# Optimization experiments

Measured on AMD Instinct MI355X. Metric: run time of the kernel, lower is better.

Reference implementation:

```python
import jax, jax.numpy as jnp
import numpy as np

DIM = 2048
BATCH = 64


def setup_inputs() -> dict:
    key = jax.random.key(0)
    kx, kq, kk, kv = jax.random.split(key, 4)
    s = 1.0 / np.sqrt(DIM).astype(np.float32)  # keep q*k logits O(1)
    x = jax.random.normal(kx, (BATCH, DIM), dtype=jnp.float32)
    Wq = jax.random.normal(kq, (DIM, DIM), dtype=jnp.float32) * s
    Wk = jax.random.normal(kk, (DIM, DIM), dtype=jnp.float32) * s
    Wv = jax.random.normal(kv, (DIM, DIM), dtype=jnp.float32) * s
    return {"x": x, "Wq": Wq, "Wk": Wk, "Wv": Wv}


def reference(x, Wq, Wk, Wv):
    # nn.Linear(dim, inner_dim, bias=False): y = x @ W.T, W: [inner_dim, dim]
    q = x @ Wq.T  # [b, N]  (head_dim = 1, so each token's q is a scalar)
    k = x @ Wk.T  # [b, N]
    v = x @ Wv.T  # [b, N]
    # dot[b,i,j] = q[b,i] * k[b,j]  (rank-1 outer product per batch)
    logits = q[:, :, None] * k[:, None, :]  # [b, N, N]
    attn = jax.nn.softmax(logits, axis=-1)
    out = jnp.einsum("bij,bj->bi", attn, v)  # [b, N]
    # dim == inner_dim -> scale is Identity
    return out
```

## Files before the change

### kernel.cpp

```cpp
#include <hip/hip_runtime.h>
#include <hip/hip_bf16.h>

#define DIM 2048
#define NB  64
#define KSL 4
#define JSL 8

typedef short bf16x8 __attribute__((ext_vector_type(8)));
typedef short s16x4  __attribute__((ext_vector_type(4)));
typedef float f32x4  __attribute__((ext_vector_type(4)));
typedef float f32x2  __attribute__((ext_vector_type(2)));

__device__ __forceinline__ unsigned short f32_to_bf16_rne(float f) {
  unsigned u = __builtin_bit_cast(unsigned, f);
  unsigned r = u + 0x7FFF + ((u >> 16) & 1);
  return (unsigned short)(r >> 16);
}

__global__ __launch_bounds__(256)
void prep(const float* __restrict__ x, unsigned short* __restrict__ xrh,
          unsigned short* __restrict__ xrl) {
  const int tg = blockIdx.x * 256 + threadIdx.x;
  const int b = tg >> 9;
  const int k = (tg & 511) * 4;
  float4 f = *(const float4*)(x + (size_t)b * DIM + k);
  const int mt = b >> 4, l15 = b & 15;
  const int ck = k >> 5, quad = (k >> 3) & 3, u = k & 7;
  const size_t off = (((size_t)(mt * 64 + ck) * 64) + quad * 16 + l15) * 8 + u;
  float vf[4] = {f.x, f.y, f.z, f.w};
  ushort4 h4, l4;
  unsigned short* hp = &h4.x;
  unsigned short* lp = &l4.x;
#pragma unroll
  for (int e = 0; e < 4; ++e) {
    unsigned short h = f32_to_bf16_rne(vf[e]);
    float hf = __builtin_bit_cast(float, ((unsigned)h) << 16);
    hp[e] = h;
    lp[e] = f32_to_bf16_rne(vf[e] - hf);
  }
  *(ushort4*)(xrh + off) = h4;
  *(ushort4*)(xrl + off) = l4;
}

#define WSTR 260

__device__ __forceinline__ void conv_store_w(short (*wh)[WSTR], short (*wl)[WSTR],
                                             const float4* wreg, int wave, int lane) {
#pragma unroll
  for (int p = 0; p < 8; ++p) {
    const int r = p * 4 + wave;
    float wf[4] = {wreg[p].x, wreg[p].y, wreg[p].z, wreg[p].w};
    s16x4 h4, l4;
#pragma unroll
    for (int e = 0; e < 4; ++e) {
      unsigned uu = __builtin_bit_cast(unsigned, wf[e]);
      h4[e] = (short)(uu >> 16);
      float hf = __builtin_bit_cast(float, uu & 0xFFFF0000u);
      float res = wf[e] - hf;
      l4[e] = (short)(__builtin_bit_cast(unsigned, res) >> 16);
    }
    *(s16x4*)&wh[r][lane * 4] = h4;
    *(s16x4*)&wl[r][lane * 4] = l4;
  }
}

__global__ __launch_bounds__(256)
void qkv_mfma(const unsigned short* __restrict__ xrh,
              const unsigned short* __restrict__ xrl,
              const float* __restrict__ Wq, const float* __restrict__ Wk,
              const float* __restrict__ Wv, float* __restrict__ part) {
  const int mat = blockIdx.z;
  const float* __restrict__ W = (mat == 0) ? Wq : ((mat == 1) ? Wk : Wv);
  const int t = threadIdx.x;
  const int wave = t >> 6, lane = t & 63;
  const int l15 = lane & 15, quad = lane >> 4;
  const int j0 = blockIdx.x * 32;
  const int kb0 = blockIdx.y * 512;

  __shared__ __align__(16) short wh[32][WSTR];
  __shared__ __align__(16) short wl[32][WSTR];

  const int jh = wave & 1;
  const int mh = wave >> 1;
  const int frow = jh * 16 + l15;
  f32x4 acc[2] = {{0.f,0.f,0.f,0.f},{0.f,0.f,0.f,0.f}};

  float4 wa[8], wb[8];
#pragma unroll
  for (int p = 0; p < 8; ++p)
    wa[p] = *(const float4*)(W + (size_t)(j0 + p * 4 + wave) * DIM + kb0 + lane * 4);

#pragma unroll
  for (int c = 0; c < 2; ++c) {
    if (c == 0) conv_store_w(wh, wl, wa, wave, lane);
    else        conv_store_w(wh, wl, wb, wave, lane);
    if (c == 0) {
#pragma unroll
      for (int p = 0; p < 8; ++p)
        wb[p] = *(const float4*)(W + (size_t)(j0 + p * 4 + wave) * DIM +
                                 kb0 + 256 + lane * 4);
    }
    __syncthreads();

    const int ckb = blockIdx.y * 16 + c * 8;
#pragma unroll
    for (int kk = 0; kk < 8; ++kk) {
      bf16x8 whf, wlf;
      *(s16x4*)&whf       = *(const s16x4*)&wh[frow][kk * 32 + quad * 8];
      *(((s16x4*)&whf)+1) = *(const s16x4*)&wh[frow][kk * 32 + quad * 8 + 4];
      *(s16x4*)&wlf       = *(const s16x4*)&wl[frow][kk * 32 + quad * 8];
      *(((s16x4*)&wlf)+1) = *(const s16x4*)&wl[frow][kk * 32 + quad * 8 + 4];
      const int ck = ckb + kk;
#pragma unroll
      for (int u = 0; u < 2; ++u) {
        const int mt = mh * 2 + u;
        const size_t xo = (((size_t)(mt * 64 + ck)) * 64 + lane) * 8;
        bf16x8 ah = *(const bf16x8*)(xrh + xo);
        bf16x8 al = *(const bf16x8*)(xrl + xo);
        acc[u] = __builtin_amdgcn_mfma_f32_16x16x32_bf16(ah, whf, acc[u], 0, 0, 0);
        acc[u] = __builtin_amdgcn_mfma_f32_16x16x32_bf16(al, whf, acc[u], 0, 0, 0);
        acc[u] = __builtin_amdgcn_mfma_f32_16x16x32_bf16(ah, wlf, acc[u], 0, 0, 0);
      }
    }
    if (c == 0) __syncthreads();
  }

  float* __restrict__ pb =
      part + ((size_t)(blockIdx.y * 3 + mat) * NB) * DIM + j0 + jh * 16 + l15;
#pragma unroll
  for (int u = 0; u < 2; ++u)
#pragma unroll
    for (int r = 0; r < 4; ++r) {
      const int b = (mh * 2 + u) * 16 + quad * 4 + r;
      pb[(size_t)b * DIM] = acc[u][r];
    }
}

__global__ __launch_bounds__(256)
void attn(const float* __restrict__ part, f32x2* __restrict__ pnd) {
  const int b = blockIdx.z, js = blockIdx.y, t = threadIdx.x;
  const int i0 = blockIdx.x * 512;
  const int ia = i0 + t, ib = i0 + 256 + t;
  const int jb = js * (DIM / JSL);

  __shared__ __align__(16) float ks[DIM / JSL];
  __shared__ __align__(16) float vs[DIM / JSL];

  float kv = 0.f, vv = 0.f, qa = 0.f, qb = 0.f;
#pragma unroll
  for (int sl = 0; sl < KSL; ++sl) {
    kv += part[((size_t)(sl * 3 + 1) * NB + b) * DIM + jb + t];
    vv += part[((size_t)(sl * 3 + 2) * NB + b) * DIM + jb + t];
    qa += part[((size_t)(sl * 3 + 0) * NB + b) * DIM + ia];
    qb += part[((size_t)(sl * 3 + 0) * NB + b) * DIM + ib];
  }
  ks[t] = kv;
  vs[t] = vv;
  __syncthreads();

  const float ca = qa * 1.4426950408889634f;
  const float cb = qb * 1.4426950408889634f;
  const f32x2 ca2 = {ca, ca}, cb2 = {cb, cb};

  f32x2 na0 = {0.f,0.f}, na1 = {0.f,0.f}, da0 = {0.f,0.f}, da1 = {0.f,0.f};
  f32x2 nb0 = {0.f,0.f}, nb1 = {0.f,0.f}, db0 = {0.f,0.f}, db1 = {0.f,0.f};
#pragma unroll 4
  for (int j = 0; j < DIM / JSL; j += 8) {
    f32x2 k01 = *(const f32x2*)(ks + j);
    f32x2 k23 = *(const f32x2*)(ks + j + 2);
    f32x2 k45 = *(const f32x2*)(ks + j + 4);
    f32x2 k67 = *(const f32x2*)(ks + j + 6);
    f32x2 v01 = *(const f32x2*)(vs + j);
    f32x2 v23 = *(const f32x2*)(vs + j + 2);
    f32x2 v45 = *(const f32x2*)(vs + j + 4);
    f32x2 v67 = *(const f32x2*)(vs + j + 6);
    f32x2 p0 = ca2 * k01, p1 = ca2 * k23, p2 = ca2 * k45, p3 = ca2 * k67;
    f32x2 e0, e1, e2, e3;
    e0.x = __builtin_amdgcn_exp2f(p0.x); e0.y = __builtin_amdgcn_exp2f(p0.y);
    e1.x = __builtin_amdgcn_exp2f(p1.x); e1.y = __builtin_amdgcn_exp2f(p1.y);
    e2.x = __builtin_amdgcn_exp2f(p2.x); e2.y = __builtin_amdgcn_exp2f(p2.y);
    e3.x = __builtin_amdgcn_exp2f(p3.x); e3.y = __builtin_amdgcn_exp2f(p3.y);
    da0 += e0; da1 += e1; da0 += e2; da1 += e3;
    na0 = __builtin_elementwise_fma(e0, v01, na0);
    na1 = __builtin_elementwise_fma(e1, v23, na1);
    na0 = __builtin_elementwise_fma(e2, v45, na0);
    na1 = __builtin_elementwise_fma(e3, v67, na1);
    f32x2 r0 = cb2 * k01, r1 = cb2 * k23, r2 = cb2 * k45, r3 = cb2 * k67;
    f32x2 f0, f1, f2, f3;
    f0.x = __builtin_amdgcn_exp2f(r0.x); f0.y = __builtin_amdgcn_exp2f(r0.y);
    f1.x = __builtin_amdgcn_exp2f(r1.x); f1.y = __builtin_amdgcn_exp2f(r1.y);
    f2.x = __builtin_amdgcn_exp2f(r2.x); f2.y = __builtin_amdgcn_exp2f(r2.y);
    f3.x = __builtin_amdgcn_exp2f(r3.x); f3.y = __builtin_amdgcn_exp2f(r3.y);
    db0 += f0; db1 += f1; db0 += f2; db1 += f3;
    nb0 = __builtin_elementwise_fma(f0, v01, nb0);
    nb1 = __builtin_elementwise_fma(f1, v23, nb1);
    nb0 = __builtin_elementwise_fma(f2, v45, nb0);
    nb1 = __builtin_elementwise_fma(f3, v67, nb1);
  }
  f32x2 nda, ndb;
  nda.x = (na0.x + na0.y) + (na1.x + na1.y);
  nda.y = (da0.x + da0.y) + (da1.x + da1.y);
  ndb.x = (nb0.x + nb0.y) + (nb1.x + nb1.y);
  ndb.y = (db0.x + db0.y) + (db1.x + db1.y);
  pnd[((size_t)b * JSL + js) * DIM + ia] = nda;
  pnd[((size_t)b * JSL + js) * DIM + ib] = ndb;
}

__global__ __launch_bounds__(256)
void attn_fin(const f32x2* __restrict__ pnd, float* __restrict__ out) {
  const int b = blockIdx.y;
  const int i = blockIdx.x * 256 + threadIdx.x;
  float n = 0.f, d = 0.f;
#pragma unroll
  for (int s = 0; s < JSL; ++s) {
    f32x2 p = pnd[((size_t)b * JSL + s) * DIM + i];
    n += p.x; d += p.y;
  }
  out[(size_t)b * DIM + i] = n / d;
}

extern "C" void kernel_launch(void* const* d_in, const int* in_sizes, int n_in,
                              void* d_out, int out_size, void* d_ws, size_t ws_size,
                              hipStream_t stream) {
  const float* x  = (const float*)d_in[0];
  const float* Wq = (const float*)d_in[1];
  const float* Wk = (const float*)d_in[2];
  const float* Wv = (const float*)d_in[3];
  float* out = (float*)d_out;

  char* w = (char*)d_ws;
  unsigned short* xrh = (unsigned short*)w;
  unsigned short* xrl = (unsigned short*)(w + (512 << 10));
  float* part = (float*)(w + (1 << 20));
  f32x2* pnd  = (f32x2*)(w + (16 << 20));

  hipLaunchKernelGGL(prep, dim3(128), dim3(256), 0, stream, x, xrh, xrl);
  hipLaunchKernelGGL(qkv_mfma, dim3(64, KSL, 3), dim3(256), 0, stream,
                     xrh, xrl, Wq, Wk, Wv, part);
  hipLaunchKernelGGL(attn, dim3(4, JSL, NB), dim3(256), 0, stream, part, pnd);
  hipLaunchKernelGGL(attn_fin, dim3(8, NB), dim3(256), 0, stream, pnd, out);
}
```

Measured before the change: 130.9 us.

## Fuse attention split-j partials and finalize into single full-row kernel

Replaces the split-j attention kernel and its separate reduction kernel with one kernel where each thread handles one query i over the whole key range, holding all 2048 k/v values in shared memory. This removes the partial numerator/denominator buffer, its write and read traffic, and one kernel launch. In exchange the grid shrinks from 2048 blocks to 512, each thread does one query instead of two with a longer serial loop, and each block stages full k/v rows from the partials, so latency hiding and parallelism may drop.

```diff
diff --git a/kernel.cpp b/kernel.cpp
--- a/kernel.cpp
+++ b/kernel.cpp
@@ -4,7 +4,6 @@
 #define DIM 2048
 #define NB  64
 #define KSL 4
-#define JSL 8
 
 typedef short bf16x8 __attribute__((ext_vector_type(8)));
 typedef short s16x4  __attribute__((ext_vector_type(4)));
@@ -137,35 +136,40 @@
 }
 
 __global__ __launch_bounds__(256)
-void attn(const float* __restrict__ part, f32x2* __restrict__ pnd) {
-  const int b = blockIdx.z, js = blockIdx.y, t = threadIdx.x;
-  const int i0 = blockIdx.x * 512;
-  const int ia = i0 + t, ib = i0 + 256 + t;
-  const int jb = js * (DIM / JSL);
-
-  __shared__ __align__(16) float ks[DIM / JSL];
-  __shared__ __align__(16) float vs[DIM / JSL];
-
-  float kv = 0.f, vv = 0.f, qa = 0.f, qb = 0.f;
+void attn_fused(const float* __restrict__ part, float* __restrict__ out) {
+  const int b = blockIdx.y, t = threadIdx.x;
+  const int i = blockIdx.x * 256 + t;
+  const int j8 = t * 8;
+
+  __shared__ __align__(16) float ks[DIM];
+  __shared__ __align__(16) float vs[DIM];
+
+  float qv = 0.f;
+  f32x4 k0 = {0.f,0.f,0.f,0.f}, k1 = {0.f,0.f,0.f,0.f};
+  f32x4 v0 = {0.f,0.f,0.f,0.f}, v1 = {0.f,0.f,0.f,0.f};
 #pragma unroll
   for (int sl = 0; sl < KSL; ++sl) {
-    kv += part[((size_t)(sl * 3 + 1) * NB + b) * DIM + jb + t];
-    vv += part[((size_t)(sl * 3 + 2) * NB + b) * DIM + jb + t];
-    qa += part[((size_t)(sl * 3 + 0) * NB + b) * DIM + ia];
-    qb += part[((size_t)(sl * 3 + 0) * NB + b) * DIM + ib];
-  }
-  ks[t] = kv;
-  vs[t] = vv;
+    const float* pq = part + ((size_t)(sl * 3 + 0) * NB + b) * DIM;
+    const float* pk = part + ((size_t)(sl * 3 + 1) * NB + b) * DIM + j8;
+    const float* pv = part + ((size_t)(sl * 3 + 2) * NB + b) * DIM + j8;
+    qv += pq[i];
+    k0 += *(const f32x4*)pk;
+    k1 += *(const f32x4*)(pk + 4);
+    v0 += *(const f32x4*)pv;
+    v1 += *(const f32x4*)(pv + 4);
+  }
+  *(f32x4*)(ks + j8)     = k0;
+  *(f32x4*)(ks + j8 + 4) = k1;
+  *(f32x4*)(vs + j8)     = v0;
+  *(f32x4*)(vs + j8 + 4) = v1;
   __syncthreads();
 
-  const float ca = qa * 1.4426950408889634f;
-  const float cb = qb * 1.4426950408889634f;
-  const f32x2 ca2 = {ca, ca}, cb2 = {cb, cb};
-
-  f32x2 na0 = {0.f,0.f}, na1 = {0.f,0.f}, da0 = {0.f,0.f}, da1 = {0.f,0.f};
-  f32x2 nb0 = {0.f,0.f}, nb1 = {0.f,0.f}, db0 = {0.f,0.f}, db1 = {0.f,0.f};
+  const float c = qv * 1.4426950408889634f;
+  const f32x2 c2 = {c, c};
+
+  f32x2 n0 = {0.f,0.f}, n1 = {0.f,0.f}, d0 = {0.f,0.f}, d1 = {0.f,0.f};
 #pragma unroll 4
-  for (int j = 0; j < DIM / JSL; j += 8) {
+  for (int j = 0; j < DIM; j += 8) {
     f32x2 k01 = *(const f32x2*)(ks + j);
     f32x2 k23 = *(const f32x2*)(ks + j + 2);
     f32x2 k45 = *(const f32x2*)(ks + j + 4);
@@ -174,49 +178,21 @@
     f32x2 v23 = *(const f32x2*)(vs + j + 2);
     f32x2 v45 = *(const f32x2*)(vs + j + 4);
     f32x2 v67 = *(const f32x2*)(vs + j + 6);
-    f32x2 p0 = ca2 * k01, p1 = ca2 * k23, p2 = ca2 * k45, p3 = ca2 * k67;
+    f32x2 p0 = c2 * k01, p1 = c2 * k23, p2 = c2 * k45, p3 = c2 * k67;
     f32x2 e0, e1, e2, e3;
     e0.x = __builtin_amdgcn_exp2f(p0.x); e0.y = __builtin_amdgcn_exp2f(p0.y);
     e1.x = __builtin_amdgcn_exp2f(p1.x); e1.y = __builtin_amdgcn_exp2f(p1.y);
     e2.x = __builtin_amdgcn_exp2f(p2.x); e2.y = __builtin_amdgcn_exp2f(p2.y);
     e3.x = __builtin_amdgcn_exp2f(p3.x); e3.y = __builtin_amdgcn_exp2f(p3.y);
-    da0 += e0; da1 += e1; da0 += e2; da1 += e3;
-    na0 = __builtin_elementwise_fma(e0, v01, na0);
-    na1 = __builtin_elementwise_fma(e1, v23, na1);
-    na0 = __builtin_elementwise_fma(e2, v45, na0);
-    na1 = __builtin_elementwise_fma(e3, v67, na1);
-    f32x2 r0 = cb2 * k01, r1 = cb2 * k23, r2 = cb2 * k45, r3 = cb2 * k67;
-    f32x2 f0, f1, f2, f3;
-    f0.x = __builtin_amdgcn_exp2f(r0.x); f0.y = __builtin_amdgcn_exp2f(r0.y);
-    f1.x = __builtin_amdgcn_exp2f(r1.x); f1.y = __builtin_amdgcn_exp2f(r1.y);
-    f2.x = __builtin_amdgcn_exp2f(r2.x); f2.y = __builtin_amdgcn_exp2f(r2.y);
-    f3.x = __builtin_amdgcn_exp2f(r3.x); f3.y = __builtin_amdgcn_exp2f(r3.y);
-    db0 += f0; db1 += f1; db0 += f2; db1 += f3;
-    nb0 = __builtin_elementwise_fma(f0, v01, nb0);
-    nb1 = __builtin_elementwise_fma(f1, v23, nb1);
-    nb0 = __builtin_elementwise_fma(f2, v45, nb0);
-    nb1 = __builtin_elementwise_fma(f3, v67, nb1);
-  }
-  f32x2 nda, ndb;
-  nda.x = (na0.x + na0.y) + (na1.x + na1.y);
-  nda.y = (da0.x + da0.y) + (da1.x + da1.y);
-  ndb.x = (nb0.x + nb0.y) + (nb1.x + nb1.y);
-  ndb.y = (db0.x + db0.y) + (db1.x + db1.y);
-  pnd[((size_t)b * JSL + js) * DIM + ia] = nda;
-  pnd[((size_t)b * JSL + js) * DIM + ib] = ndb;
-}
-
-__global__ __launch_bounds__(256)
-void attn_fin(const f32x2* __restrict__ pnd, float* __restrict__ out) {
-  const int b = blockIdx.y;
-  const int i = blockIdx.x * 256 + threadIdx.x;
-  float n = 0.f, d = 0.f;
-#pragma unroll
-  for (int s = 0; s < JSL; ++s) {
-    f32x2 p = pnd[((size_t)b * JSL + s) * DIM + i];
-    n += p.x; d += p.y;
-  }
-  out[(size_t)b * DIM + i] = n / d;
+    d0 += e0; d1 += e1; d0 += e2; d1 += e3;
+    n0 = __builtin_elementwise_fma(e0, v01, n0);
+    n1 = __builtin_elementwise_fma(e1, v23, n1);
+    n0 = __builtin_elementwise_fma(e2, v45, n0);
+    n1 = __builtin_elementwise_fma(e3, v67, n1);
+  }
+  const float nn = (n0.x + n0.y) + (n1.x + n1.y);
+  const float dd = (d0.x + d0.y) + (d1.x + d1.y);
+  out[(size_t)b * DIM + i] = nn / dd;
 }
 
 extern "C" void kernel_launch(void* const* d_in, const int* in_sizes, int n_in,
@@ -232,11 +208,10 @@
   unsigned short* xrh = (unsigned short*)w;
   unsigned short* xrl = (unsigned short*)(w + (512 << 10));
   float* part = (float*)(w + (1 << 20));
-  f32x2* pnd  = (f32x2*)(w + (16 << 20));
 
   hipLaunchKernelGGL(prep, dim3(128), dim3(256), 0, stream, x, xrh, xrl);
   hipLaunchKernelGGL(qkv_mfma, dim3(64, KSL, 3), dim3(256), 0, stream,
                      xrh, xrl, Wq, Wk, Wv, part);
-  hipLaunchKernelGGL(attn, dim3(4, JSL, NB), dim3(256), 0, stream, part, pnd);
-  hipLaunchKernelGGL(attn_fin, dim3(8, NB), dim3(256), 0, stream, pnd, out);
-}
+  hipLaunchKernelGGL(attn_fused, dim3(DIM / 256, NB), dim3(256), 0, stream,
+                     part, out);
+}
```

New measurement: 135.7 us. 3.7% more time.
